# Kernel optimization log

Measured on AMD Instinct MI355X. Metric: run time of the kernel, lower is better.

## Reference

```python
import jax, jax.numpy as jnp
import numpy as np

N_NODES = 50000
N_EDGES = 800000


def graph_conv(h, W, b, src, dst, n_nodes):
    # DGL GraphConv with norm='both':
    #   out = D_in^{-1/2} * A^T * (D_out^{-1/2} * h) @ W + b
    ones = jnp.ones((src.shape[0],), dtype=h.dtype)
    deg_out = jax.ops.segment_sum(ones, src, num_segments=n_nodes)
    deg_in = jax.ops.segment_sum(ones, dst, num_segments=n_nodes)
    norm_src = jnp.clip(deg_out, 1.0) ** -0.5  # [N]
    norm_dst = jnp.clip(deg_in, 1.0) ** -0.5   # [N]
    msg = (h * norm_src[:, None])[src]          # [E, F] gather
    agg = jax.ops.segment_sum(msg, dst, num_segments=n_nodes)  # [N, F] scatter
    return (agg * norm_dst[:, None]) @ W + b


def setup_inputs() -> dict:
    key = jax.random.key(0)
    ks = jax.random.split(key, 5)
    h = jax.random.normal(ks[0], (N_NODES, 64), dtype=jnp.float32)
    src = jax.random.randint(ks[1], (N_EDGES,), 0, N_NODES, dtype=jnp.int32)
    dst = jax.random.randint(ks[2], (N_EDGES,), 0, N_NODES, dtype=jnp.int32)
    W1 = jax.random.normal(ks[3], (64, 128), dtype=jnp.float32) * (1.0 / np.sqrt(64))
    b1 = jnp.zeros((128,), dtype=jnp.float32)
    W2 = jax.random.normal(ks[4], (128, 64), dtype=jnp.float32) * (1.0 / np.sqrt(128))
    b2 = jnp.zeros((64,), dtype=jnp.float32)
    return {"h": h, "src": src, "dst": dst, "W1": W1, "b1": b1, "W2": W2, "b2": b2}


def reference(h, src, dst, W1, b1, W2, b2):
    n = h.shape[0]
    h1 = jax.nn.relu(graph_conv(h, W1, b1, src, dst, n))
    out = graph_conv(h1, W2, b2, src, dst, n)
    return out
```

## Files before the change

kernel.cpp:

```cpp
#include <hip/hip_runtime.h>


#define NBMAX 512
#define CAPLOG 12
#define CAP (1 << CAPLOG)

typedef __attribute__((ext_vector_type(8))) short bf16x8;
typedef __attribute__((ext_vector_type(4))) float f32x4;

__device__ inline unsigned short f2bf(float f) {
    unsigned int u = __float_as_uint(f);
    unsigned int r = (u + 0x7FFFu + ((u >> 16) & 1u)) >> 16;
    return (unsigned short)r;
}
__device__ inline float bf2f_lo(unsigned int u) { return __uint_as_float(u << 16); }
__device__ inline float bf2f_hi(unsigned int u) { return __uint_as_float(u & 0xFFFF0000u); }
__device__ inline float bf2f(unsigned short h) {
    return __uint_as_float((unsigned int)h << 16);
}

__global__ __launch_bounds__(256) void place_direct(const int* __restrict__ src,
        const int* __restrict__ dst, int* __restrict__ cnt_s, int* __restrict__ cnt_d,
        unsigned char* __restrict__ ss, unsigned int* __restrict__ sd,
        int n_edges, int nb) {
    __shared__ int hs[NBMAX], hd[NBMAX], bs[NBMAX], bd[NBMAX];
    for (int i = threadIdx.x; i < nb; i += 256) { hs[i] = 0; hd[i] = 0; }
    __syncthreads();
    int chunk = (n_edges + gridDim.x - 1) / gridDim.x;
    int e0 = blockIdx.x * chunk;
    int e1 = e0 + chunk; if (e1 > n_edges) e1 = n_edges;
    for (int e = e0 + (int)threadIdx.x; e < e1; e += 256) {
        atomicAdd(&hs[src[e] >> 7], 1);
        atomicAdd(&hd[dst[e] >> 7], 1);
    }
    __syncthreads();
    for (int i = threadIdx.x; i < nb; i += 256) {
        int v = hs[i]; bs[i] = v ? atomicAdd(&cnt_s[i], v) : 0; hs[i] = 0;
        v = hd[i];     bd[i] = v ? atomicAdd(&cnt_d[i], v) : 0; hd[i] = 0;
    }
    __syncthreads();
    for (int e = e0 + (int)threadIdx.x; e < e1; e += 256) {
        int s = src[e], d = dst[e];
        int sb = s >> 7, db = d >> 7;
        int ps = bs[sb] + atomicAdd(&hs[sb], 1);
        ss[((size_t)sb << CAPLOG) + ps] = (unsigned char)(s & 127);
        int pd = bd[db] + atomicAdd(&hd[db], 1);
        sd[((size_t)db << CAPLOG) + pd] = ((unsigned int)(d & 127) << 25) | (unsigned int)s;
    }
}

__global__ __launch_bounds__(256) void prep(const float* __restrict__ h,
        const unsigned char* __restrict__ ss, const int* __restrict__ cnt_s,
        const unsigned int* __restrict__ sd, const int* __restrict__ cnt_d,
        float* __restrict__ norm_src, unsigned short* __restrict__ xb,
        int2* __restrict__ node_rng, unsigned short* __restrict__ srt,
        float* __restrict__ norm_dst, int n) {
    __shared__ int cnt[128], cur[128];
    __shared__ float nrm[128];
    __shared__ int w0tot;
    const int b = blockIdx.x;
    const int tid = threadIdx.x;

    if (tid < 128) cnt[tid] = 0;
    __syncthreads();
    {
        int used = cnt_s[b];
        const unsigned char* p = ss + ((size_t)b << CAPLOG);
        for (int i = tid; i < used; i += 256) atomicAdd(&cnt[p[i]], 1);
    }
    __syncthreads();
    if (tid < 128) {
        int c = cnt[tid]; if (c < 1) c = 1;
        float s = 1.0f / sqrtf((float)c);
        nrm[tid] = s;
        int node = (b << 7) + tid;
        if (node < n) norm_src[node] = s;
    }
    __syncthreads();
    {
        int base = b << 7;
        for (int t = tid; t < 128 * 16; t += 256) {
            int r = t >> 4, c4 = (t & 15) << 2;
            int node = base + r;
            if (node < n) {
                float s = nrm[r];
                float4 v = *(const float4*)(h + (size_t)node * 64 + c4);
                ushort4 o;
                o.x = f2bf(v.x * s); o.y = f2bf(v.y * s);
                o.z = f2bf(v.z * s); o.w = f2bf(v.w * s);
                *(ushort4*)(xb + (size_t)node * 64 + c4) = o;
            }
        }
    }
    __syncthreads();

    if (tid < 128) cnt[tid] = 0;
    __syncthreads();
    int used = cnt_d[b];
    const unsigned int* p = sd + ((size_t)b << CAPLOG);
    for (int i = tid; i < used; i += 256) atomicAdd(&cnt[p[i] >> 25], 1);
    __syncthreads();
    int lane = tid & 63, wid = tid >> 6;
    int v = (tid < 128) ? cnt[tid] : 0;
    int incl = v;
    #pragma unroll
    for (int d = 1; d < 64; d <<= 1) {
        int t = __shfl_up(incl, d, 64);
        if (lane >= d) incl += t;
    }
    if (tid == 63) w0tot = incl;
    __syncthreads();
    if (tid < 128) {
        int excl = incl - v + (wid == 1 ? w0tot : 0);
        cur[tid] = excl;
        int node = (b << 7) + tid;
        if (node < n) {
            int base = b << CAPLOG;
            node_rng[node] = make_int2(base + excl, base + excl + v);
            int c = v; if (c < 1) c = 1;
            norm_dst[node] = 1.0f / sqrtf((float)c);
        }
    }
    __syncthreads();
    for (int i = tid; i < used; i += 256) {
        unsigned int e = p[i];
        int l = (int)(e >> 25);
        int pos = atomicAdd(&cur[l], 1);
        srt[((size_t)b << CAPLOG) + pos] = (unsigned short)(e & 0xFFFFu);
    }
}

__global__ __launch_bounds__(256) void gather24(const unsigned short* __restrict__ xb,
        const unsigned short* __restrict__ srt, const int2* __restrict__ node_rng,
        const float* __restrict__ nrm, const float* __restrict__ bias,
        void* __restrict__ outp, int write_bf, int n_nodes) {
    int node = blockIdx.x * 4 + (threadIdx.x >> 6);
    if (node >= n_nodes) return;
    int lane = threadIdx.x & 63;
    int g  = lane >> 3;
    int c8 = (lane & 7) * 8;
    int2 rng = node_rng[node];
    int a0 = rng.x, a1 = rng.y;
    float acc[8];
    #pragma unroll
    for (int j = 0; j < 8; ++j) acc[j] = 0.f;
    for (int base = a0; base < a1; base += 24) {
        #pragma unroll
        for (int u = 0; u < 3; ++u) {
            int ei = base + u * 8 + g;
            int idx = ei < a1 ? ei : a1 - 1;
            float msk = ei < a1 ? 1.0f : 0.0f;
            int s = srt[idx];
            const uint4 v = *(const uint4*)(xb + (size_t)s * 64 + c8);
            acc[0] = fmaf(bf2f_lo(v.x), msk, acc[0]);
            acc[1] = fmaf(bf2f_hi(v.x), msk, acc[1]);
            acc[2] = fmaf(bf2f_lo(v.y), msk, acc[2]);
            acc[3] = fmaf(bf2f_hi(v.y), msk, acc[3]);
            acc[4] = fmaf(bf2f_lo(v.z), msk, acc[4]);
            acc[5] = fmaf(bf2f_hi(v.z), msk, acc[5]);
            acc[6] = fmaf(bf2f_lo(v.w), msk, acc[6]);
            acc[7] = fmaf(bf2f_hi(v.w), msk, acc[7]);
        }
    }
    #pragma unroll
    for (int off = 8; off < 64; off <<= 1) {
        #pragma unroll
        for (int j = 0; j < 8; ++j) acc[j] += __shfl_xor(acc[j], off, 64);
    }
    if (g == 0) {
        float s = nrm[node];
        float r[8];
        #pragma unroll
        for (int j = 0; j < 8; ++j) r[j] = acc[j] * s;
        if (write_bf) {
            unsigned short rb[8];
            #pragma unroll
            for (int j = 0; j < 8; ++j) rb[j] = f2bf(r[j]);
            unsigned short* o = (unsigned short*)outp + (size_t)node * 64 + c8;
            *(ushort4*)(o)     = make_ushort4(rb[0], rb[1], rb[2], rb[3]);
            *(ushort4*)(o + 4) = make_ushort4(rb[4], rb[5], rb[6], rb[7]);
        } else {
            if (bias) {
                #pragma unroll
                for (int j = 0; j < 8; ++j) r[j] += bias[c8 + j];
            }
            float* o = (float*)outp + (size_t)node * 64 + c8;
            *(float4*)(o)     = make_float4(r[0], r[1], r[2], r[3]);
            *(float4*)(o + 4) = make_float4(r[4], r[5], r[6], r[7]);
        }
    }
}

__global__ __launch_bounds__(256) void gemm12(const unsigned short* __restrict__ Ab,
        const float* __restrict__ W1, const float* __restrict__ b1,
        const float* __restrict__ norm, const float* __restrict__ W2,
        unsigned short* __restrict__ y2b, int n) {
    __shared__ unsigned short W1t[128 * 72];
    __shared__ unsigned short W2t[64 * 136];
    __shared__ unsigned short Hs[64 * 136];
    __shared__ float b1s[128];
    const int tid = threadIdx.x;

    for (int i = tid; i < 8192; i += 256) {
        int k = i >> 7, nn = i & 127;
        W1t[nn * 72 + k] = f2bf(W1[i]);
    }
    for (int i = tid; i < 8192; i += 256) {
        int k = i >> 6, nn = i & 63;
        W2t[nn * 136 + k] = f2bf(W2[i]);
    }
    if (tid < 128) b1s[tid] = b1[tid];
    __syncthreads();

    const int w  = tid >> 6;
    const int l  = tid & 63;
    const int ln = l & 15;
    const int q  = l >> 4;
    const int m0 = blockIdx.x * 64 + w * 16;

    int arow = m0 + ln; if (arow > n - 1) arow = n - 1;
    const unsigned short* arp = Ab + (size_t)arow * 64 + q * 8;
    bf16x8 a0 = *(const bf16x8*)(arp);
    bf16x8 a1 = *(const bf16x8*)(arp + 32);

    float ns[4];
    #pragma unroll
    for (int r = 0; r < 4; ++r) {
        int node = m0 + q * 4 + r;
        ns[r] = norm[node < n ? node : n - 1];
    }

    #pragma unroll
    for (int c = 0; c < 8; ++c) {
        const unsigned short* bp = W1t + (c * 16 + ln) * 72 + q * 8;
        bf16x8 b0 = *(const bf16x8*)(bp);
        bf16x8 bk = *(const bf16x8*)(bp + 32);
        f32x4 acc = {0.f, 0.f, 0.f, 0.f};
        acc = __builtin_amdgcn_mfma_f32_16x16x32_bf16(a0, b0, acc, 0, 0, 0);
        acc = __builtin_amdgcn_mfma_f32_16x16x32_bf16(a1, bk, acc, 0, 0, 0);
        int col = c * 16 + ln;
        float bb = b1s[col];
        #pragma unroll
        for (int r = 0; r < 4; ++r) {
            float v = acc[r] + bb;
            v = v > 0.f ? v : 0.f;
            Hs[(w * 16 + q * 4 + r) * 136 + col] = f2bf(v * ns[r]);
        }
    }
    __syncthreads();

    const unsigned short* hp = Hs + (size_t)(w * 16 + ln) * 136 + q * 8;
    bf16x8 h0 = *(const bf16x8*)(hp);
    bf16x8 h1 = *(const bf16x8*)(hp + 32);
    bf16x8 h2 = *(const bf16x8*)(hp + 64);
    bf16x8 h3 = *(const bf16x8*)(hp + 96);
    #pragma unroll
    for (int c = 0; c < 4; ++c) {
        const unsigned short* bp = W2t + (c * 16 + ln) * 136 + q * 8;
        f32x4 acc = {0.f, 0.f, 0.f, 0.f};
        acc = __builtin_amdgcn_mfma_f32_16x16x32_bf16(h0, *(const bf16x8*)(bp),      acc, 0, 0, 0);
        acc = __builtin_amdgcn_mfma_f32_16x16x32_bf16(h1, *(const bf16x8*)(bp + 32), acc, 0, 0, 0);
        acc = __builtin_amdgcn_mfma_f32_16x16x32_bf16(h2, *(const bf16x8*)(bp + 64), acc, 0, 0, 0);
        acc = __builtin_amdgcn_mfma_f32_16x16x32_bf16(h3, *(const bf16x8*)(bp + 96), acc, 0, 0, 0);
        #pragma unroll
        for (int r = 0; r < 4; ++r) {
            int node = m0 + q * 4 + r;
            if (node < n)
                y2b[(size_t)node * 64 + c * 16 + ln] = f2bf(acc[r]);
        }
    }
}

extern "C" void kernel_launch(void* const* d_in, const int* in_sizes, int n_in,
                              void* d_out, int out_size, void* d_ws, size_t ws_size,
                              hipStream_t stream) {
    const float* h   = (const float*)d_in[0];
    const int*   src = (const int*)d_in[1];
    const int*   dst = (const int*)d_in[2];
    const float* W1  = (const float*)d_in[3];
    const float* b1  = (const float*)d_in[4];
    const float* W2  = (const float*)d_in[5];
    const float* b2  = (const float*)d_in[6];
    float* out = (float*)d_out;

    const int n = in_sizes[0] / 64;
    const int E = in_sizes[1];
    const int nb = (n + 127) >> 7;

    char* p = (char*)d_ws;
    auto alloc = [&](size_t bytes) {
        void* r = (void*)p;
        p += (bytes + 255) & ~(size_t)255;
        return r;
    };
    float* norm_src      = (float*)alloc((size_t)n * 4);
    float* norm_dst      = (float*)alloc((size_t)n * 4);
    int2* node_rng       = (int2*)alloc((size_t)n * 8);
    int* cnt2            = (int*)alloc((size_t)2 * nb * 4);
    int* cnt_s = cnt2;
    int* cnt_d = cnt2 + nb;
    unsigned int* sd     = (unsigned int*)alloc((size_t)nb * CAP * 4);
    unsigned short* xb   = (unsigned short*)alloc((size_t)n * 64 * 2);
    unsigned short* agg1b= (unsigned short*)alloc((size_t)n * 64 * 2);
    unsigned short* y2b  = (unsigned short*)alloc((size_t)n * 64 * 2);
    unsigned short* srt  = (unsigned short*)alloc((size_t)nb * CAP * 2);
    unsigned char* ssb   = (unsigned char*)alloc((size_t)nb * CAP);

    hipMemsetAsync(cnt2, 0, 2 * (size_t)nb * sizeof(int), stream);

    place_direct<<<256, 256, 0, stream>>>(src, dst, cnt_s, cnt_d, ssb, sd, E, nb);
    prep<<<nb, 256, 0, stream>>>(h, ssb, cnt_s, sd, cnt_d, norm_src, xb,
                                 node_rng, srt, norm_dst, n);

    int gb = (n + 3) / 4;
    gather24<<<gb, 256, 0, stream>>>(xb, srt, node_rng, norm_dst, nullptr,
                                     (void*)agg1b, 1, n);

    int tb = (n + 63) / 64;
    gemm12<<<tb, 256, 0, stream>>>(agg1b, W1, b1, norm_src, W2, y2b, n);

    gather24<<<gb, 256, 0, stream>>>(y2b, srt, node_rng, norm_dst, b2,
                                     (void*)out, 0, n);
}
```

Before: 170.2 us.

## Pre-convert weights once, cache edge indices in LDS, widen place grid

The last block of the placement kernel now converts W1/W2 to transposed, padded bf16 once into global scratch. The gemm kernel then copies those with 16-byte loads instead of every block redoing the fp32-to-bf16 transpose. The placement kernel also caches each block's src/dst edge slice in shared memory so the second pass avoids re-reading global memory. It launches about 500 blocks of 1600 edges instead of 256 larger chunks, which adds more global counter atomics and extra shared memory per block.

```diff
diff --git a/kernel.cpp b/kernel.cpp
--- a/kernel.cpp
+++ b/kernel.cpp
@@ -4,6 +4,7 @@
 #define NBMAX 512
 #define CAPLOG 12
 #define CAP (1 << CAPLOG)
+#define ECACHE 1600
 
 typedef __attribute__((ext_vector_type(8))) short bf16x8;
 typedef __attribute__((ext_vector_type(4))) float f32x4;
@@ -22,16 +23,34 @@
 __global__ __launch_bounds__(256) void place_direct(const int* __restrict__ src,
         const int* __restrict__ dst, int* __restrict__ cnt_s, int* __restrict__ cnt_d,
         unsigned char* __restrict__ ss, unsigned int* __restrict__ sd,
-        int n_edges, int nb) {
+        int n_edges, int nb,
+        const float* __restrict__ W1, const float* __restrict__ W2,
+        unsigned short* __restrict__ w1t_g, unsigned short* __restrict__ w2t_g) {
+    if (blockIdx.x == gridDim.x - 1) {
+        for (int i = threadIdx.x; i < 8192; i += 256) {
+            int k = i >> 7, nn = i & 127;
+            w1t_g[nn * 72 + k] = f2bf(W1[i]);
+        }
+        for (int i = threadIdx.x; i < 8192; i += 256) {
+            int k = i >> 6, nn = i & 63;
+            w2t_g[nn * 136 + k] = f2bf(W2[i]);
+        }
+        return;
+    }
     __shared__ int hs[NBMAX], hd[NBMAX], bs[NBMAX], bd[NBMAX];
+    __shared__ int es[ECACHE], ed[ECACHE];
     for (int i = threadIdx.x; i < nb; i += 256) { hs[i] = 0; hd[i] = 0; }
-    __syncthreads();
-    int chunk = (n_edges + gridDim.x - 1) / gridDim.x;
-    int e0 = blockIdx.x * chunk;
-    int e1 = e0 + chunk; if (e1 > n_edges) e1 = n_edges;
-    for (int e = e0 + (int)threadIdx.x; e < e1; e += 256) {
-        atomicAdd(&hs[src[e] >> 7], 1);
-        atomicAdd(&hd[dst[e] >> 7], 1);
+    int e0 = blockIdx.x * ECACHE;
+    int e1 = e0 + ECACHE; if (e1 > n_edges) e1 = n_edges;
+    int m = e1 - e0;
+    for (int i = threadIdx.x; i < m; i += 256) {
+        es[i] = src[e0 + i];
+        ed[i] = dst[e0 + i];
+    }
+    __syncthreads();
+    for (int i = threadIdx.x; i < m; i += 256) {
+        atomicAdd(&hs[es[i] >> 7], 1);
+        atomicAdd(&hd[ed[i] >> 7], 1);
     }
     __syncthreads();
     for (int i = threadIdx.x; i < nb; i += 256) {
@@ -39,8 +58,8 @@
         v = hd[i];     bd[i] = v ? atomicAdd(&cnt_d[i], v) : 0; hd[i] = 0;
     }
     __syncthreads();
-    for (int e = e0 + (int)threadIdx.x; e < e1; e += 256) {
-        int s = src[e], d = dst[e];
+    for (int i = threadIdx.x; i < m; i += 256) {
+        int s = es[i], d = ed[i];
         int sb = s >> 7, db = d >> 7;
         int ps = bs[sb] + atomicAdd(&hs[sb], 1);
         ss[((size_t)sb << CAPLOG) + ps] = (unsigned char)(s & 127);
@@ -192,22 +211,22 @@
 }
 
 __global__ __launch_bounds__(256) void gemm12(const unsigned short* __restrict__ Ab,
-        const float* __restrict__ W1, const float* __restrict__ b1,
-        const float* __restrict__ norm, const float* __restrict__ W2,
+        const unsigned short* __restrict__ w1t_g, const float* __restrict__ b1,
+        const float* __restrict__ norm, const unsigned short* __restrict__ w2t_g,
         unsigned short* __restrict__ y2b, int n) {
-    __shared__ unsigned short W1t[128 * 72];
-    __shared__ unsigned short W2t[64 * 136];
-    __shared__ unsigned short Hs[64 * 136];
+    __shared__ __align__(16) unsigned short W1t[128 * 72];
+    __shared__ __align__(16) unsigned short W2t[64 * 136];
+    __shared__ __align__(16) unsigned short Hs[64 * 136];
     __shared__ float b1s[128];
     const int tid = threadIdx.x;
 
-    for (int i = tid; i < 8192; i += 256) {
-        int k = i >> 7, nn = i & 127;
-        W1t[nn * 72 + k] = f2bf(W1[i]);
-    }
-    for (int i = tid; i < 8192; i += 256) {
-        int k = i >> 6, nn = i & 63;
-        W2t[nn * 136 + k] = f2bf(W2[i]);
+    {
+        const uint4* s1 = (const uint4*)w1t_g;
+        uint4* d1 = (uint4*)W1t;
+        for (int i = tid; i < 1152; i += 256) d1[i] = s1[i];
+        const uint4* s2 = (const uint4*)w2t_g;
+        uint4* d2 = (uint4*)W2t;
+        for (int i = tid; i < 1088; i += 256) d2[i] = s2[i];
     }
     if (tid < 128) b1s[tid] = b1[tid];
     __syncthreads();
@@ -305,10 +324,14 @@
     unsigned short* y2b  = (unsigned short*)alloc((size_t)n * 64 * 2);
     unsigned short* srt  = (unsigned short*)alloc((size_t)nb * CAP * 2);
     unsigned char* ssb   = (unsigned char*)alloc((size_t)nb * CAP);
+    unsigned short* w1t_g= (unsigned short*)alloc((size_t)128 * 72 * 2);
+    unsigned short* w2t_g= (unsigned short*)alloc((size_t)64 * 136 * 2);
 
     hipMemsetAsync(cnt2, 0, 2 * (size_t)nb * sizeof(int), stream);
 
-    place_direct<<<256, 256, 0, stream>>>(src, dst, cnt_s, cnt_d, ssb, sd, E, nb);
+    int nbe = (E + ECACHE - 1) / ECACHE;
+    place_direct<<<nbe + 1, 256, 0, stream>>>(src, dst, cnt_s, cnt_d, ssb, sd,
+                                              E, nb, W1, W2, w1t_g, w2t_g);
     prep<<<nb, 256, 0, stream>>>(h, ssb, cnt_s, sd, cnt_d, norm_src, xb,
                                  node_rng, srt, norm_dst, n);
 
@@ -317,7 +340,7 @@
                                      (void*)agg1b, 1, n);
 
     int tb = (n + 63) / 64;
-    gemm12<<<tb, 256, 0, stream>>>(agg1b, W1, b1, norm_src, W2, y2b, n);
+    gemm12<<<tb, 256, 0, stream>>>(agg1b, w1t_g, b1, norm_src, w2t_g, y2b, n);
 
     gather24<<<gb, 256, 0, stream>>>(y2b, srt, node_rng, norm_dst, b2,
                                      (void*)out, 0, n);
```

Measured after the change: 182.6 us. 1.07x slower.
